# Performance work log

Measured on AMD Instinct MI355X. Metric: run time of the kernel, lower is better.

## Reference

```python
import jax, jax.numpy as jnp
import numpy as np

NUM_BUCKETS = 64
MAX_DISTANCE = 50000.0


def setup_inputs() -> dict:
    R, I, N, E, H = 64, 512, 4, 256, 8
    key = jax.random.key(0)
    ks = jax.random.split(key, 12)
    p = lambda k, shape: (jax.random.normal(k, shape, dtype=jnp.float32) * 0.02)
    return {
        "x": jax.random.normal(ks[0], (R, I, N, E), dtype=jnp.float32),
        "distances": jax.random.randint(ks[1], (N, I, I), 0, 50000).astype(jnp.int32),
        "Wq": p(ks[2], (E, E)), "bq": jnp.zeros((E,), jnp.float32),
        "Wk": p(ks[3], (E, E)), "bk": jnp.zeros((E,), jnp.float32),
        "Wv": p(ks[4], (E, E)), "bv": jnp.zeros((E,), jnp.float32),
        "Wo": p(ks[5], (E, E)), "bo": jnp.zeros((E,), jnp.float32),
        "rel_emb": p(ks[6], (NUM_BUCKETS, H)),
    }


def reference(x, distances, Wq, bq, Wk, bk, Wv, bv, Wo, bo, rel_emb):
    R, I, N, E = x.shape
    H = rel_emb.shape[1]
    D = E // H
    # scaling = head_dim**-0.5 / sqrt(num_rows)
    scaling = (D ** -0.5) / np.sqrt(R)

    def proj(W, b):
        return (jnp.einsum('rine,fe->rinf', x, W) + b).reshape(R, I, N, H, D)

    q = proj(Wq, bq) * scaling
    k = proj(Wk, bk)
    v = proj(Wv, bv)

    # Row-summed attention logits: (H, N, I, J)
    attn_weights = jnp.einsum('rinhd,rjnhd->hnij', q, k)

    # T5-style relative position bias (buckets = linspace boundaries)
    buckets = jnp.linspace(0.0, MAX_DISTANCE, NUM_BUCKETS - 1)
    abs_dist = jnp.abs(distances).astype(jnp.float32)
    # torch.bucketize(right=False) == searchsorted side='left'
    bucket_idx = jnp.searchsorted(buckets, abs_dist, side='left')  # (N, I, J)
    bias = rel_emb[bucket_idx]                  # (N, I, J, H)
    attn_weights = attn_weights + jnp.transpose(bias, (3, 0, 1, 2))

    attn_probs = jax.nn.softmax(attn_weights, axis=-1)  # dropout p=0.0 -> identity

    context = jnp.einsum('hnij,rjnhd->rinhd', attn_probs, v).reshape(R, I, N, E)
    output = jnp.einsum('rine,fe->rinf', context, Wo) + bo
    return output, attn_probs
```

## Files before the change

### kernel.cpp

```cpp
#include <hip/hip_runtime.h>

typedef unsigned short u16;
typedef unsigned int u32;
typedef float f32x4 __attribute__((ext_vector_type(4)));
typedef short bf16x8 __attribute__((ext_vector_type(8)));
typedef unsigned short u16x8 __attribute__((ext_vector_type(8)));

#define SL 33554432u

__device__ __forceinline__ float bf2f(u16 u) {
  u32 v = ((u32)u) << 16;
  return __builtin_bit_cast(float, v);
}
__device__ __forceinline__ u16 f2bf(float f) {
  u32 i = __builtin_bit_cast(u32, f);
  i += 0x7fffu + ((i >> 16) & 1u);
  return (u16)(i >> 16);
}

#define GLDS16(g, l) __builtin_amdgcn_global_load_lds( \
    (const __attribute__((address_space(1))) void*)(g), \
    (__attribute__((address_space(3))) void*)(l), 16, 0, 0)

__device__ __forceinline__ void stage128(const u16* gbase, int ldk, u16* lds, int tid) {
  #pragma unroll
  for (int rep = 0; rep < 4; ++rep) {
    int c = tid + rep * 256;
    int row = c >> 3, slot = c & 7;
    const u16* g = gbase + (size_t)row * ldk + ((slot ^ (row & 7)) << 3);
    GLDS16(g, lds + c * 8);
  }
}

__device__ __forceinline__ void mfma128(const u16* As, const u16* Bs, int lane,
                                        int wm0, int wn0, f32x4 acc[4][4]) {
  #pragma unroll
  for (int kk = 0; kk < 2; ++kk) {
    bf16x8 a[4], b[4];
    #pragma unroll
    for (int mi = 0; mi < 4; ++mi) {
      int r = wm0 + mi * 16 + (lane & 15);
      int c16 = (kk * 4 + (lane >> 4)) ^ (r & 7);
      a[mi] = *(const bf16x8*)(As + r * 64 + c16 * 8);
    }
    #pragma unroll
    for (int ni = 0; ni < 4; ++ni) {
      int r = wn0 + ni * 16 + (lane & 15);
      int c16 = (kk * 4 + (lane >> 4)) ^ (r & 7);
      b[ni] = *(const bf16x8*)(Bs + r * 64 + c16 * 8);
    }
    #pragma unroll
    for (int mi = 0; mi < 4; ++mi)
      #pragma unroll
      for (int ni = 0; ni < 4; ++ni)
        acc[mi][ni] = __builtin_amdgcn_mfma_f32_16x16x32_bf16(a[mi], b[ni], acc[mi][ni], 0, 0, 0);
  }
}

__device__ __forceinline__ void gemm_core(const u16* A, int ldkA, const u16* B, int ldkB,
                                          int NT, u16* As, u16* Bs,
                                          int tid, int lane, int wm0, int wn0,
                                          f32x4 acc[4][4]) {
  for (int t = 0; t < NT; ++t) {
    stage128(A + t * 64, ldkA, As, tid);
    stage128(B + t * 64, ldkB, Bs, tid);
    __syncthreads();
    mfma128(As, Bs, lane, wm0, wn0, acc);
    __syncthreads();
  }
}

__device__ __forceinline__ void stage128_512(const u16* gbase, int ldk, u16* lds, int tid) {
  #pragma unroll
  for (int rep = 0; rep < 2; ++rep) {
    int c = tid + rep * 512;
    int row = c >> 3, slot = c & 7;
    const u16* g = gbase + (size_t)row * ldk + ((slot ^ (row & 7)) << 3);
    GLDS16(g, lds + c * 8);
  }
}

__device__ __forceinline__ void mfma128_8w(const u16* As, const u16* Bs, int lane,
                                           int wm0, int wn0, f32x4 acc[4][2]) {
  #pragma unroll
  for (int kk = 0; kk < 2; ++kk) {
    bf16x8 a[4], b[2];
    #pragma unroll
    for (int mi = 0; mi < 4; ++mi) {
      int r = wm0 + mi * 16 + (lane & 15);
      int c16 = (kk * 4 + (lane >> 4)) ^ (r & 7);
      a[mi] = *(const bf16x8*)(As + r * 64 + c16 * 8);
    }
    #pragma unroll
    for (int ni = 0; ni < 2; ++ni) {
      int r = wn0 + ni * 16 + (lane & 15);
      int c16 = (kk * 4 + (lane >> 4)) ^ (r & 7);
      b[ni] = *(const bf16x8*)(Bs + r * 64 + c16 * 8);
    }
    #pragma unroll
    for (int mi = 0; mi < 4; ++mi)
      #pragma unroll
      for (int ni = 0; ni < 2; ++ni)
        acc[mi][ni] = __builtin_amdgcn_mfma_f32_16x16x32_bf16(a[mi], b[ni], acc[mi][ni], 0, 0, 0);
  }
}

__device__ __forceinline__ void gemm_core_512(const u16* A, int ldkA, const u16* B, int ldkB,
                                              int NT, u16* As, u16* Bs,
                                              int tid, int lane, int wm0, int wn0,
                                              f32x4 acc[4][2]) {
  for (int t = 0; t < NT; ++t) {
    stage128_512(A + t * 64, ldkA, As, tid);
    stage128_512(B + t * 64, ldkB, Bs, tid);
    __syncthreads();
    mfma128_8w(As, Bs, lane, wm0, wn0, acc);
    __syncthreads();
  }
}

__global__ __launch_bounds__(256) void k_castx(const float* __restrict__ src,
                                               u16* __restrict__ dst) {
  int idx = blockIdx.x * 256 + threadIdx.x;
  const float4* s = (const float4*)src;
  float4 a = s[(size_t)idx * 2], b = s[(size_t)idx * 2 + 1];
  u16x8 o;
  o[0] = f2bf(a.x); o[1] = f2bf(a.y); o[2] = f2bf(a.z); o[3] = f2bf(a.w);
  o[4] = f2bf(b.x); o[5] = f2bf(b.y); o[6] = f2bf(b.z); o[7] = f2bf(b.w);
  *(u16x8*)(dst + (size_t)idx * 8) = o;
}

__global__ __launch_bounds__(256) void k_castw(
    const float* __restrict__ Wq, const float* __restrict__ Wk,
    const float* __restrict__ Wv, const float* __restrict__ Wo,
    u16* __restrict__ Wb) {
  int idx = blockIdx.x * 256 + threadIdx.x;
  int w = idx >> 13, off = idx & 8191;
  const float* src = (w == 0) ? Wq : (w == 1) ? Wk : (w == 2) ? Wv : Wo;
  const float4* s = (const float4*)(src + (size_t)off * 8);
  float4 a = s[0], b = s[1];
  u16x8 o;
  o[0] = f2bf(a.x); o[1] = f2bf(a.y); o[2] = f2bf(a.z); o[3] = f2bf(a.w);
  o[4] = f2bf(b.x); o[5] = f2bf(b.y); o[6] = f2bf(b.z); o[7] = f2bf(b.w);
  *(u16x8*)(Wb + (size_t)w * 65536 + (size_t)off * 8) = o;
}

__global__ __launch_bounds__(512) void k_proj_mm(
    const u16* __restrict__ xb, const u16* __restrict__ Wb,
    const float* __restrict__ bq, const float* __restrict__ bk, const float* __restrict__ bv,
    u16* __restrict__ qt, u16* __restrict__ kt, u16* __restrict__ vt, float scaling) {
  __shared__ __align__(16) u16 As[128 * 64];
  __shared__ __align__(16) u16 Bs[128 * 64];
  const int tid = threadIdx.x, lane = tid & 63, wave = tid >> 6;
  const int wm0 = (wave >> 2) * 64, wn0 = (wave & 3) * 32;
  const int m0 = blockIdx.x * 128, n0 = blockIdx.y * 128, w = blockIdx.z;

  f32x4 acc[4][2];
  #pragma unroll
  for (int mi = 0; mi < 4; ++mi)
    #pragma unroll
    for (int ni = 0; ni < 2; ++ni) acc[mi][ni] = (f32x4){0.f, 0.f, 0.f, 0.f};

  gemm_core_512(xb + (size_t)m0 * 256, 256, Wb + w * 65536 + (size_t)n0 * 256, 256,
                4, As, Bs, tid, lane, wm0, wn0, acc);

  const float* bias = (w == 0) ? bq : (w == 1) ? bk : bv;
  u16* dst = (w == 0) ? qt : (w == 1) ? kt : vt;
  const float sc = (w == 0) ? scaling : 1.0f;

  #pragma unroll
  for (int mi = 0; mi < 4; ++mi)
    #pragma unroll
    for (int ni = 0; ni < 2; ++ni) {
      int f = n0 + wn0 + ni * 16 + (lane & 15);
      int h = f >> 5, d = f & 31;
      float bb = bias[f];
      #pragma unroll
      for (int q = 0; q < 4; ++q) {
        int m = m0 + wm0 + mi * 16 + (lane >> 4) * 4 + q;
        int n = m & 3, i = (m >> 2) & 511, r = m >> 11;
        size_t o = ((size_t)((n * 8 + h) * 512 + i)) * 2048 + r * 32 + d;
        dst[o] = f2bf((acc[mi][ni][q] + bb) * sc);
      }
    }
}

__global__ __launch_bounds__(512) void k_attn_mm(
    const u16* __restrict__ qt, const u16* __restrict__ kt, u16* __restrict__ lgt) {
  __shared__ __align__(16) u16 As[128 * 64];
  __shared__ __align__(16) u16 Bs[128 * 64];
  const int tid = threadIdx.x, lane = tid & 63, wave = tid >> 6;
  const int wm0 = (wave >> 2) * 64, wn0 = (wave & 3) * 32;
  const int bid = blockIdx.x;
  const int sb = (bid & 7) * 64 + (bid >> 3);
  const int nh = sb >> 4, tt = sb & 15;
  const int m0 = (tt >> 2) * 128, n0 = (tt & 3) * 128;

  f32x4 acc[4][2];
  #pragma unroll
  for (int mi = 0; mi < 4; ++mi)
    #pragma unroll
    for (int ni = 0; ni < 2; ++ni) acc[mi][ni] = (f32x4){0.f, 0.f, 0.f, 0.f};

  const size_t base = (size_t)nh * 512 * 2048;
  gemm_core_512(qt + base + (size_t)m0 * 2048, 2048, kt + base + (size_t)n0 * 2048, 2048,
                32, As, Bs, tid, lane, wm0, wn0, acc);

  #pragma unroll
  for (int mi = 0; mi < 4; ++mi)
    #pragma unroll
    for (int ni = 0; ni < 2; ++ni) {
      int col = n0 + wn0 + ni * 16 + (lane & 15);
      #pragma unroll
      for (int q = 0; q < 4; ++q) {
        int row = m0 + wm0 + mi * 16 + (lane >> 4) * 4 + q;
        lgt[(size_t)nh * 262144 + (size_t)row * 512 + col] = f2bf(acc[mi][ni][q]);
      }
    }
}

__global__ __launch_bounds__(256) void k_softmax(
    const u16* __restrict__ lgt, const int* __restrict__ dist, const float* __restrict__ rel,
    float* __restrict__ probs, u16* __restrict__ pbf) {
  const int t = threadIdx.x;
  const int lane = t & 63, wv = t >> 6;
  const int b = blockIdx.x;
  const int i = b & 511, n = b >> 9;

  const int* dr = dist + ((size_t)n * 512 + i) * 512 + lane * 8;
  int4 dA = *(const int4*)dr, dB = *(const int4*)(dr + 4);
  int dd[8] = {dA.x, dA.y, dA.z, dA.w, dB.x, dB.y, dB.z, dB.w};
  int u[8];
  #pragma unroll
  for (int j = 0; j < 8; ++j) {
    int v = dd[j] < 0 ? -dd[j] : dd[j];
    int q = (62 * v + 49999) / 50000; if (q > 63) q = 63;
    u[j] = q;
  }

  #pragma unroll
  for (int hh = 0; hh < 2; ++hh) {
    const int h = wv * 2 + hh;
    const int nh = n * 8 + h;
    const u16* lr = lgt + ((size_t)nh * 512 + i) * 512 + lane * 8;
    u16x8 L = *(const u16x8*)lr;
    float vj[8];
    float mx = -1e30f;
    #pragma unroll
    for (int j = 0; j < 8; ++j) {
      vj[j] = bf2f(L[j]) + rel[u[j] * 8 + h];
      mx = fmaxf(mx, vj[j]);
    }
    #pragma unroll
    for (int off = 32; off; off >>= 1) mx = fmaxf(mx, __shfl_xor(mx, off));
    float s = 0.f;
    #pragma unroll
    for (int j = 0; j < 8; ++j) { vj[j] = __expf(vj[j] - mx); s += vj[j]; }
    #pragma unroll
    for (int off = 32; off; off >>= 1) s += __shfl_xor(s, off);
    float inv = 1.0f / s;
    float4 pa, pb;
    pa.x = vj[0]*inv; pa.y = vj[1]*inv; pa.z = vj[2]*inv; pa.w = vj[3]*inv;
    pb.x = vj[4]*inv; pb.y = vj[5]*inv; pb.z = vj[6]*inv; pb.w = vj[7]*inv;
    size_t po = ((size_t)(h * 4 + n) * 512 + i) * 512 + lane * 8;
    *(float4*)(probs + po) = pa;
    *(float4*)(probs + po + 4) = pb;
    u16x8 pc;
    pc[0]=f2bf(pa.x); pc[1]=f2bf(pa.y); pc[2]=f2bf(pa.z); pc[3]=f2bf(pa.w);
    pc[4]=f2bf(pb.x); pc[5]=f2bf(pb.y); pc[6]=f2bf(pb.z); pc[7]=f2bf(pb.w);
    size_t pq = ((size_t)nh * 512 + i) * 512 + lane * 8;
    *(u16x8*)(pbf + pq) = pc;
  }
}

__global__ __launch_bounds__(256) void k_vtrans(const u16* __restrict__ vt, u16* __restrict__ vtt) {
  __shared__ u16 ts[64][72];
  const int b = blockIdx.x;
  const int ct_ = b & 31, it = (b >> 5) & 7, nh = b >> 8;
  const int i0 = it * 64, c0 = ct_ * 64;
  const int t = threadIdx.x;
  #pragma unroll
  for (int rep = 0; rep < 2; ++rep) {
    int c = t + rep * 256;
    int r = c >> 3, q = c & 7;
    u16x8 v = *(const u16x8*)(vt + ((size_t)nh * 512 + i0 + r) * 2048 + c0 + q * 8);
    #pragma unroll
    for (int j = 0; j < 8; ++j) ts[r][q * 8 + j] = v[j];
  }
  __syncthreads();
  #pragma unroll
  for (int rep = 0; rep < 2; ++rep) {
    int c = t + rep * 256;
    int rr = c >> 3, q = c & 7;
    u16x8 o;
    #pragma unroll
    for (int j = 0; j < 8; ++j) o[j] = ts[q * 8 + j][rr];
    *(u16x8*)(vtt + ((size_t)nh * 2048 + c0 + rr) * 512 + i0 + q * 8) = o;
  }
}

__global__ __launch_bounds__(256) void k_ctx_mm(
    const u16* __restrict__ vtt, const u16* __restrict__ pbf, u16* __restrict__ ct) {
  __shared__ __align__(16) u16 lds[16640];
  u16* As = lds;
  u16* Bs = lds + 8192;
  u16* ts = lds;
  const int tid = threadIdx.x, lane = tid & 63, wave = tid >> 6;
  const int wm0 = (wave >> 1) * 64, wn0 = (wave & 1) * 64;
  const int bid = blockIdx.x;
  const int sb = (bid & 7) * 256 + (bid >> 3);
  const int nh = sb >> 6, tt = sb & 63;
  const int m0 = (tt >> 2) * 128, n0 = (tt & 3) * 128;
  const int n = nh >> 3, h = nh & 7;

  f32x4 acc[4][4];
  #pragma unroll
  for (int mi = 0; mi < 4; ++mi)
    #pragma unroll
    for (int ni = 0; ni < 4; ++ni) acc[mi][ni] = (f32x4){0.f, 0.f, 0.f, 0.f};

  gemm_core(vtt + (size_t)nh * 1048576 + (size_t)m0 * 512, 512,
            pbf + (size_t)nh * 262144 + (size_t)n0 * 512, 512,
            8, As, Bs, tid, lane, wm0, wn0, acc);

  #pragma unroll
  for (int mi = 0; mi < 4; ++mi)
    #pragma unroll
    for (int ni = 0; ni < 4; ++ni) {
      int i_l = wn0 + ni * 16 + (lane & 15);
      #pragma unroll
      for (int q = 0; q < 4; ++q) {
        int c_l = wm0 + mi * 16 + (lane >> 4) * 4 + q;
        ts[i_l * 130 + c_l] = f2bf(acc[mi][ni][q]);
      }
    }
  __syncthreads();
  #pragma unroll
  for (int cc = 0; cc < 2; ++cc) {
    int ch = tid + cc * 256;
    int i_l = ch & 127, r_l = ch >> 7;
    const u16* src = ts + i_l * 130 + r_l * 32;
    int rr = (m0 >> 5) + r_l;
    size_t o = ((size_t)((rr * 512 + n0 + i_l) * 4 + n)) * 256 + h * 32;
    #pragma unroll
    for (int j = 0; j < 4; ++j)
      *(u16x8*)(ct + o + j * 8) = *(const u16x8*)(src + j * 8);
  }
}

__global__ __launch_bounds__(256) void k_oproj_mm(
    const u16* __restrict__ ct, const u16* __restrict__ Wob,
    const float* __restrict__ bo, float* __restrict__ out) {
  __shared__ __align__(16) u16 As[128 * 64];
  __shared__ __align__(16) u16 Bs[128 * 64];
  const int tid = threadIdx.x, lane = tid & 63, wave = tid >> 6;
  const int wm0 = (wave >> 1) * 64, wn0 = (wave & 1) * 64;
  const int bid = blockIdx.x;
  const int sb = (bid & 7) * 256 + (bid >> 3);
  const int m0 = (sb >> 1) * 128, n0 = (sb & 1) * 128;

  f32x4 acc[4][4];
  #pragma unroll
  for (int mi = 0; mi < 4; ++mi)
    #pragma unroll
    for (int ni = 0; ni < 4; ++ni) acc[mi][ni] = (f32x4){0.f, 0.f, 0.f, 0.f};

  gemm_core(ct + (size_t)m0 * 256, 256, Wob + (size_t)n0 * 256, 256,
            4, As, Bs, tid, lane, wm0, wn0, acc);

  #pragma unroll
  for (int mi = 0; mi < 4; ++mi)
    #pragma unroll
    for (int ni = 0; ni < 4; ++ni) {
      int col = n0 + wn0 + ni * 16 + (lane & 15);
      float bb = bo[col];
      #pragma unroll
      for (int q = 0; q < 4; ++q) {
        int row = m0 + wm0 + mi * 16 + (lane >> 4) * 4 + q;
        out[(size_t)row * 256 + col] = acc[mi][ni][q] + bb;
      }
    }
}

extern "C" void kernel_launch(void* const* d_in, const int* in_sizes, int n_in,
                              void* d_out, int out_size, void* d_ws, size_t ws_size,
                              hipStream_t stream) {
  const float* x  = (const float*)d_in[0];
  const int* dist = (const int*)d_in[1];
  const float* Wq = (const float*)d_in[2];
  const float* bq = (const float*)d_in[3];
  const float* Wk = (const float*)d_in[4];
  const float* bk = (const float*)d_in[5];
  const float* Wv = (const float*)d_in[6];
  const float* bv = (const float*)d_in[7];
  const float* Wo = (const float*)d_in[8];
  const float* bo = (const float*)d_in[9];
  const float* rel = (const float*)d_in[10];
  float* out = (float*)d_out;
  float* probs = out + (size_t)SL;

  u16* ws = (u16*)d_ws;
  u16* xb  = ws;
  u16* qt  = ws + (size_t)SL;
  u16* kt  = ws + (size_t)2 * SL;
  u16* vt  = ws + (size_t)3 * SL;
  u16* lgt = xb;
  u16* pbf = qt;
  u16* vtt = kt;
  u16* ctb = xb;
  u16* Wb  = ws + (size_t)4 * SL;

  const float scaling = 0.022097086912079608f;

  k_castx  <<<16384, 256, 0, stream>>>(x, xb);
  k_castw  <<<128, 256, 0, stream>>>(Wq, Wk, Wv, Wo, Wb);
  k_proj_mm<<<dim3(1024, 2, 3), 512, 0, stream>>>(xb, Wb, bq, bk, bv, qt, kt, vt, scaling);
  k_attn_mm<<<512, 512, 0, stream>>>(qt, kt, lgt);
  k_softmax<<<2048, 256, 0, stream>>>(lgt, dist, rel, probs, pbf);
  k_vtrans <<<8192, 256, 0, stream>>>(vt, vtt);
  k_ctx_mm <<<2048, 256, 0, stream>>>(vtt, pbf, ctb);
  k_oproj_mm<<<2048, 256, 0, stream>>>(ctb, Wb + 196608, bo, out);
}
```

Measured before the change: 358.6 us.

## Fuse x cast into projection GEMM and double-buffer all GEMM mainloops

Removes the separate fp32-to-bf16 cast kernel for x: the projection GEMM now loads fp32 x directly, converts it in registers and writes it to LDS. It also adds an L2-friendly block swizzle. All GEMM kernels (projection, attention logits, context, output projection) switch to double-buffered LDS with one barrier per k-step, so global loads overlap MFMA work. The context and output GEMMs move from 256 to 512 threads with 8 waves. The cost is twice the LDS per block, which can reduce occupancy, and register-staged x loads whose latency must hide behind the MFMAs.

```diff
diff --git a/kernel.cpp b/kernel.cpp
--- a/kernel.cpp
+++ b/kernel.cpp
@@ -22,54 +22,6 @@
     (const __attribute__((address_space(1))) void*)(g), \
     (__attribute__((address_space(3))) void*)(l), 16, 0, 0)
 
-__device__ __forceinline__ void stage128(const u16* gbase, int ldk, u16* lds, int tid) {
-  #pragma unroll
-  for (int rep = 0; rep < 4; ++rep) {
-    int c = tid + rep * 256;
-    int row = c >> 3, slot = c & 7;
-    const u16* g = gbase + (size_t)row * ldk + ((slot ^ (row & 7)) << 3);
-    GLDS16(g, lds + c * 8);
-  }
-}
-
-__device__ __forceinline__ void mfma128(const u16* As, const u16* Bs, int lane,
-                                        int wm0, int wn0, f32x4 acc[4][4]) {
-  #pragma unroll
-  for (int kk = 0; kk < 2; ++kk) {
-    bf16x8 a[4], b[4];
-    #pragma unroll
-    for (int mi = 0; mi < 4; ++mi) {
-      int r = wm0 + mi * 16 + (lane & 15);
-      int c16 = (kk * 4 + (lane >> 4)) ^ (r & 7);
-      a[mi] = *(const bf16x8*)(As + r * 64 + c16 * 8);
-    }
-    #pragma unroll
-    for (int ni = 0; ni < 4; ++ni) {
-      int r = wn0 + ni * 16 + (lane & 15);
-      int c16 = (kk * 4 + (lane >> 4)) ^ (r & 7);
-      b[ni] = *(const bf16x8*)(Bs + r * 64 + c16 * 8);
-    }
-    #pragma unroll
-    for (int mi = 0; mi < 4; ++mi)
-      #pragma unroll
-      for (int ni = 0; ni < 4; ++ni)
-        acc[mi][ni] = __builtin_amdgcn_mfma_f32_16x16x32_bf16(a[mi], b[ni], acc[mi][ni], 0, 0, 0);
-  }
-}
-
-__device__ __forceinline__ void gemm_core(const u16* A, int ldkA, const u16* B, int ldkB,
-                                          int NT, u16* As, u16* Bs,
-                                          int tid, int lane, int wm0, int wn0,
-                                          f32x4 acc[4][4]) {
-  for (int t = 0; t < NT; ++t) {
-    stage128(A + t * 64, ldkA, As, tid);
-    stage128(B + t * 64, ldkB, Bs, tid);
-    __syncthreads();
-    mfma128(As, Bs, lane, wm0, wn0, acc);
-    __syncthreads();
-  }
-}
-
 __device__ __forceinline__ void stage128_512(const u16* gbase, int ldk, u16* lds, int tid) {
   #pragma unroll
   for (int rep = 0; rep < 2; ++rep) {
@@ -103,30 +55,6 @@
       for (int ni = 0; ni < 2; ++ni)
         acc[mi][ni] = __builtin_amdgcn_mfma_f32_16x16x32_bf16(a[mi], b[ni], acc[mi][ni], 0, 0, 0);
   }
-}
-
-__device__ __forceinline__ void gemm_core_512(const u16* A, int ldkA, const u16* B, int ldkB,
-                                              int NT, u16* As, u16* Bs,
-                                              int tid, int lane, int wm0, int wn0,
-                                              f32x4 acc[4][2]) {
-  for (int t = 0; t < NT; ++t) {
-    stage128_512(A + t * 64, ldkA, As, tid);
-    stage128_512(B + t * 64, ldkB, Bs, tid);
-    __syncthreads();
-    mfma128_8w(As, Bs, lane, wm0, wn0, acc);
-    __syncthreads();
-  }
-}
-
-__global__ __launch_bounds__(256) void k_castx(const float* __restrict__ src,
-                                               u16* __restrict__ dst) {
-  int idx = blockIdx.x * 256 + threadIdx.x;
-  const float4* s = (const float4*)src;
-  float4 a = s[(size_t)idx * 2], b = s[(size_t)idx * 2 + 1];
-  u16x8 o;
-  o[0] = f2bf(a.x); o[1] = f2bf(a.y); o[2] = f2bf(a.z); o[3] = f2bf(a.w);
-  o[4] = f2bf(b.x); o[5] = f2bf(b.y); o[6] = f2bf(b.z); o[7] = f2bf(b.w);
-  *(u16x8*)(dst + (size_t)idx * 8) = o;
 }
 
 __global__ __launch_bounds__(256) void k_castw(
@@ -145,14 +73,23 @@
 }
 
 __global__ __launch_bounds__(512) void k_proj_mm(
-    const u16* __restrict__ xb, const u16* __restrict__ Wb,
+    const float* __restrict__ x, const u16* __restrict__ Wb,
     const float* __restrict__ bq, const float* __restrict__ bk, const float* __restrict__ bv,
     u16* __restrict__ qt, u16* __restrict__ kt, u16* __restrict__ vt, float scaling) {
-  __shared__ __align__(16) u16 As[128 * 64];
-  __shared__ __align__(16) u16 Bs[128 * 64];
+  __shared__ __align__(16) u16 lds[32768];
   const int tid = threadIdx.x, lane = tid & 63, wave = tid >> 6;
   const int wm0 = (wave >> 2) * 64, wn0 = (wave & 3) * 32;
-  const int m0 = blockIdx.x * 128, n0 = blockIdx.y * 128, w = blockIdx.z;
+  const int bid = blockIdx.x;
+  const int sb = (bid & 7) * 768 + (bid >> 3);
+  const int mt = sb / 6, g = sb % 6;
+  const int m0 = mt * 128, n0 = (g & 1) * 128, w = g >> 1;
+
+  const int c0 = tid, c1 = tid + 512;
+  const int row0 = c0 >> 3, slot0 = c0 & 7;
+  const int row1 = c1 >> 3, slot1 = c1 & 7;
+  const float* a0p = x + (size_t)(m0 + row0) * 256 + ((slot0 ^ (row0 & 7)) << 3);
+  const float* a1p = x + (size_t)(m0 + row1) * 256 + ((slot1 ^ (row1 & 7)) << 3);
+  const u16* Bw = Wb + w * 65536 + (size_t)n0 * 256;
 
   f32x4 acc[4][2];
   #pragma unroll
@@ -160,8 +97,42 @@
     #pragma unroll
     for (int ni = 0; ni < 2; ++ni) acc[mi][ni] = (f32x4){0.f, 0.f, 0.f, 0.f};
 
-  gemm_core_512(xb + (size_t)m0 * 256, 256, Wb + w * 65536 + (size_t)n0 * 256, 256,
-                4, As, Bs, tid, lane, wm0, wn0, acc);
+  {
+    float4 va0 = *(const float4*)a0p, vb0 = *(const float4*)(a0p + 4);
+    float4 va1 = *(const float4*)a1p, vb1 = *(const float4*)(a1p + 4);
+    u16x8 o0, o1;
+    o0[0]=f2bf(va0.x); o0[1]=f2bf(va0.y); o0[2]=f2bf(va0.z); o0[3]=f2bf(va0.w);
+    o0[4]=f2bf(vb0.x); o0[5]=f2bf(vb0.y); o0[6]=f2bf(vb0.z); o0[7]=f2bf(vb0.w);
+    o1[0]=f2bf(va1.x); o1[1]=f2bf(va1.y); o1[2]=f2bf(va1.z); o1[3]=f2bf(va1.w);
+    o1[4]=f2bf(vb1.x); o1[5]=f2bf(vb1.y); o1[6]=f2bf(vb1.z); o1[7]=f2bf(vb1.w);
+    *(u16x8*)(lds + c0 * 8) = o0;
+    *(u16x8*)(lds + c1 * 8) = o1;
+    stage128_512(Bw, 256, lds + 16384, tid);
+  }
+  __syncthreads();
+
+  for (int t = 0; t < 4; ++t) {
+    const int cur = t & 1, nxt = cur ^ 1;
+    float4 va0, vb0, va1, vb1;
+    if (t < 3) {
+      va0 = *(const float4*)(a0p + (t + 1) * 64);
+      vb0 = *(const float4*)(a0p + (t + 1) * 64 + 4);
+      va1 = *(const float4*)(a1p + (t + 1) * 64);
+      vb1 = *(const float4*)(a1p + (t + 1) * 64 + 4);
+      stage128_512(Bw + (t + 1) * 64, 256, lds + 16384 + nxt * 8192, tid);
+    }
+    mfma128_8w(lds + cur * 8192, lds + 16384 + cur * 8192, lane, wm0, wn0, acc);
+    if (t < 3) {
+      u16x8 o0, o1;
+      o0[0]=f2bf(va0.x); o0[1]=f2bf(va0.y); o0[2]=f2bf(va0.z); o0[3]=f2bf(va0.w);
+      o0[4]=f2bf(vb0.x); o0[5]=f2bf(vb0.y); o0[6]=f2bf(vb0.z); o0[7]=f2bf(vb0.w);
+      o1[0]=f2bf(va1.x); o1[1]=f2bf(va1.y); o1[2]=f2bf(va1.z); o1[3]=f2bf(va1.w);
+      o1[4]=f2bf(vb1.x); o1[5]=f2bf(vb1.y); o1[6]=f2bf(vb1.z); o1[7]=f2bf(vb1.w);
+      *(u16x8*)(lds + nxt * 8192 + c0 * 8) = o0;
+      *(u16x8*)(lds + nxt * 8192 + c1 * 8) = o1;
+    }
+    __syncthreads();
+  }
 
   const float* bias = (w == 0) ? bq : (w == 1) ? bk : bv;
   u16* dst = (w == 0) ? qt : (w == 1) ? kt : vt;
@@ -186,8 +157,8 @@
 
 __global__ __launch_bounds__(512) void k_attn_mm(
     const u16* __restrict__ qt, const u16* __restrict__ kt, u16* __restrict__ lgt) {
-  __shared__ __align__(16) u16 As[128 * 64];
-  __shared__ __align__(16) u16 Bs[128 * 64];
+  __shared__ __align__(16) u16 As[2][8192];
+  __shared__ __align__(16) u16 Bs[2][8192];
   const int tid = threadIdx.x, lane = tid & 63, wave = tid >> 6;
   const int wm0 = (wave >> 2) * 64, wn0 = (wave & 3) * 32;
   const int bid = blockIdx.x;
@@ -202,8 +173,21 @@
     for (int ni = 0; ni < 2; ++ni) acc[mi][ni] = (f32x4){0.f, 0.f, 0.f, 0.f};
 
   const size_t base = (size_t)nh * 512 * 2048;
-  gemm_core_512(qt + base + (size_t)m0 * 2048, 2048, kt + base + (size_t)n0 * 2048, 2048,
-                32, As, Bs, tid, lane, wm0, wn0, acc);
+  const u16* A = qt + base + (size_t)m0 * 2048;
+  const u16* B = kt + base + (size_t)n0 * 2048;
+
+  stage128_512(A, 2048, As[0], tid);
+  stage128_512(B, 2048, Bs[0], tid);
+  __syncthreads();
+  for (int t = 0; t < 32; ++t) {
+    int cur = t & 1;
+    if (t + 1 < 32) {
+      stage128_512(A + (t + 1) * 64, 2048, As[cur ^ 1], tid);
+      stage128_512(B + (t + 1) * 64, 2048, Bs[cur ^ 1], tid);
+    }
+    mfma128_8w(As[cur], Bs[cur], lane, wm0, wn0, acc);
+    __syncthreads();
+  }
 
   #pragma unroll
   for (int mi = 0; mi < 4; ++mi)
@@ -298,34 +282,44 @@
   }
 }
 
-__global__ __launch_bounds__(256) void k_ctx_mm(
+__global__ __launch_bounds__(512) void k_ctx_mm(
     const u16* __restrict__ vtt, const u16* __restrict__ pbf, u16* __restrict__ ct) {
-  __shared__ __align__(16) u16 lds[16640];
-  u16* As = lds;
-  u16* Bs = lds + 8192;
+  __shared__ __align__(16) u16 lds[32768];
   u16* ts = lds;
   const int tid = threadIdx.x, lane = tid & 63, wave = tid >> 6;
-  const int wm0 = (wave >> 1) * 64, wn0 = (wave & 1) * 64;
+  const int wm0 = (wave >> 2) * 64, wn0 = (wave & 3) * 32;
   const int bid = blockIdx.x;
   const int sb = (bid & 7) * 256 + (bid >> 3);
   const int nh = sb >> 6, tt = sb & 63;
   const int m0 = (tt >> 2) * 128, n0 = (tt & 3) * 128;
   const int n = nh >> 3, h = nh & 7;
 
-  f32x4 acc[4][4];
-  #pragma unroll
-  for (int mi = 0; mi < 4; ++mi)
-    #pragma unroll
-    for (int ni = 0; ni < 4; ++ni) acc[mi][ni] = (f32x4){0.f, 0.f, 0.f, 0.f};
-
-  gemm_core(vtt + (size_t)nh * 1048576 + (size_t)m0 * 512, 512,
-            pbf + (size_t)nh * 262144 + (size_t)n0 * 512, 512,
-            8, As, Bs, tid, lane, wm0, wn0, acc);
-
-  #pragma unroll
-  for (int mi = 0; mi < 4; ++mi)
-    #pragma unroll
-    for (int ni = 0; ni < 4; ++ni) {
+  f32x4 acc[4][2];
+  #pragma unroll
+  for (int mi = 0; mi < 4; ++mi)
+    #pragma unroll
+    for (int ni = 0; ni < 2; ++ni) acc[mi][ni] = (f32x4){0.f, 0.f, 0.f, 0.f};
+
+  const u16* A = vtt + (size_t)nh * 1048576 + (size_t)m0 * 512;
+  const u16* B = pbf + (size_t)nh * 262144 + (size_t)n0 * 512;
+
+  stage128_512(A, 512, lds, tid);
+  stage128_512(B, 512, lds + 16384, tid);
+  __syncthreads();
+  for (int t = 0; t < 8; ++t) {
+    int cur = t & 1;
+    if (t + 1 < 8) {
+      stage128_512(A + (t + 1) * 64, 512, lds + (cur ^ 1) * 8192, tid);
+      stage128_512(B + (t + 1) * 64, 512, lds + 16384 + (cur ^ 1) * 8192, tid);
+    }
+    mfma128_8w(lds + cur * 8192, lds + 16384 + cur * 8192, lane, wm0, wn0, acc);
+    __syncthreads();
+  }
+
+  #pragma unroll
+  for (int mi = 0; mi < 4; ++mi)
+    #pragma unroll
+    for (int ni = 0; ni < 2; ++ni) {
       int i_l = wn0 + ni * 16 + (lane & 15);
       #pragma unroll
       for (int q = 0; q < 4; ++q) {
@@ -334,9 +328,8 @@
       }
     }
   __syncthreads();
-  #pragma unroll
-  for (int cc = 0; cc < 2; ++cc) {
-    int ch = tid + cc * 256;
+  {
+    int ch = tid;
     int i_l = ch & 127, r_l = ch >> 7;
     const u16* src = ts + i_l * 130 + r_l * 32;
     int rr = (m0 >> 5) + r_l;
@@ -347,30 +340,42 @@
   }
 }
 
-__global__ __launch_bounds__(256) void k_oproj_mm(
+__global__ __launch_bounds__(512) void k_oproj_mm(
     const u16* __restrict__ ct, const u16* __restrict__ Wob,
     const float* __restrict__ bo, float* __restrict__ out) {
-  __shared__ __align__(16) u16 As[128 * 64];
-  __shared__ __align__(16) u16 Bs[128 * 64];
+  __shared__ __align__(16) u16 lds[32768];
   const int tid = threadIdx.x, lane = tid & 63, wave = tid >> 6;
-  const int wm0 = (wave >> 1) * 64, wn0 = (wave & 1) * 64;
+  const int wm0 = (wave >> 2) * 64, wn0 = (wave & 3) * 32;
   const int bid = blockIdx.x;
   const int sb = (bid & 7) * 256 + (bid >> 3);
   const int m0 = (sb >> 1) * 128, n0 = (sb & 1) * 128;
 
-  f32x4 acc[4][4];
-  #pragma unroll
-  for (int mi = 0; mi < 4; ++mi)
-    #pragma unroll
-    for (int ni = 0; ni < 4; ++ni) acc[mi][ni] = (f32x4){0.f, 0.f, 0.f, 0.f};
-
-  gemm_core(ct + (size_t)m0 * 256, 256, Wob + (size_t)n0 * 256, 256,
-            4, As, Bs, tid, lane, wm0, wn0, acc);
-
-  #pragma unroll
-  for (int mi = 0; mi < 4; ++mi)
-    #pragma unroll
-    for (int ni = 0; ni < 4; ++ni) {
+  f32x4 acc[4][2];
+  #pragma unroll
+  for (int mi = 0; mi < 4; ++mi)
+    #pragma unroll
+    for (int ni = 0; ni < 2; ++ni) acc[mi][ni] = (f32x4){0.f, 0.f, 0.f, 0.f};
+
+  const u16* A = ct + (size_t)m0 * 256;
+  const u16* B = Wob + (size_t)n0 * 256;
+
+  stage128_512(A, 256, lds, tid);
+  stage128_512(B, 256, lds + 16384, tid);
+  __syncthreads();
+  for (int t = 0; t < 4; ++t) {
+    int cur = t & 1;
+    if (t + 1 < 4) {
+      stage128_512(A + (t + 1) * 64, 256, lds + (cur ^ 1) * 8192, tid);
+      stage128_512(B + (t + 1) * 64, 256, lds + 16384 + (cur ^ 1) * 8192, tid);
+    }
+    mfma128_8w(lds + cur * 8192, lds + 16384 + cur * 8192, lane, wm0, wn0, acc);
+    __syncthreads();
+  }
+
+  #pragma unroll
+  for (int mi = 0; mi < 4; ++mi)
+    #pragma unroll
+    for (int ni = 0; ni < 2; ++ni) {
       int col = n0 + wn0 + ni * 16 + (lane & 15);
       float bb = bo[col];
       #pragma unroll
@@ -399,24 +404,22 @@
   float* probs = out + (size_t)SL;
 
   u16* ws = (u16*)d_ws;
-  u16* xb  = ws;
+  u16* lgt = ws;
   u16* qt  = ws + (size_t)SL;
   u16* kt  = ws + (size_t)2 * SL;
   u16* vt  = ws + (size_t)3 * SL;
-  u16* lgt = xb;
   u16* pbf = qt;
   u16* vtt = kt;
-  u16* ctb = xb;
+  u16* ctb = lgt;
   u16* Wb  = ws + (size_t)4 * SL;
 
   const float scaling = 0.022097086912079608f;
 
-  k_castx  <<<16384, 256, 0, stream>>>(x, xb);
   k_castw  <<<128, 256, 0, stream>>>(Wq, Wk, Wv, Wo, Wb);
-  k_proj_mm<<<dim3(1024, 2, 3), 512, 0, stream>>>(xb, Wb, bq, bk, bv, qt, kt, vt, scaling);
+  k_proj_mm<<<6144, 512, 0, stream>>>(x, Wb, bq, bk, bv, qt, kt, vt, scaling);
   k_attn_mm<<<512, 512, 0, stream>>>(qt, kt, lgt);
   k_softmax<<<2048, 256, 0, stream>>>(lgt, dist, rel, probs, pbf);
   k_vtrans <<<8192, 256, 0, stream>>>(vt, vtt);
-  k_ctx_mm <<<2048, 256, 0, stream>>>(vtt, pbf, ctb);
-  k_oproj_mm<<<2048, 256, 0, stream>>>(ctb, Wb + 196608, bo, out);
-}
+  k_ctx_mm <<<2048, 512, 0, stream>>>(vtt, pbf, ctb);
+  k_oproj_mm<<<2048, 512, 0, stream>>>(ctb, Wb + 196608, bo, out);
+}
```

Result: slower. 378.3 us (+5.5%).
